# Kernel tuning notes

Measured on AMD Instinct MI355X. Metric: run time of the kernel, lower is better.

Reference implementation:

```python
import jax, jax.numpy as jnp
import numpy as np

B, T, C, H = 256, 256, 384, 64
MAX_REL = 3  # max_relative_position hardcoded in module


def setup_inputs() -> dict:
    key = jax.random.key(0)
    ks = jax.random.split(key, 6)
    s = 1.0 / np.sqrt(C)
    return {
        "x": jax.random.normal(ks[0], (B, T, C), dtype=jnp.float32),
        "Wq": jax.random.normal(ks[1], (C, H), dtype=jnp.float32) * s,
        "Wk": jax.random.normal(ks[2], (C, H), dtype=jnp.float32) * s,
        "Wv": jax.random.normal(ks[3], (C, H), dtype=jnp.float32) * s,
        "rel_k_table": jax.random.normal(ks[4], (2 * MAX_REL + 1, H), dtype=jnp.float32) * s,
        "rel_v_table": jax.random.normal(ks[5], (2 * MAX_REL + 1, H), dtype=jnp.float32) * s,
    }


def reference(x, Wq, Wk, Wv, rel_k_table, rel_v_table):
    Bd, Td, Cd = x.shape
    Hd = Wq.shape[1]
    q = x @ Wq  # [B,T,H]
    k = x @ Wk
    v = x @ Wv
    # relative position indices, clipped Shaw-style
    r = jnp.arange(Td)
    idx = jnp.clip(r[None, :] - r[:, None], -MAX_REL, MAX_REL) + MAX_REL  # [T,T]
    rk = rel_k_table[idx]  # [T,T,H]
    rv = rel_v_table[idx]  # [T,T,H]
    attn1 = jnp.einsum('bth,bsh->bts', q, k)
    attn2 = jnp.einsum('bth,tsh->bts', q, rk)
    scale = jnp.sqrt(jnp.asarray(Hd, dtype=x.dtype))
    scores = (attn1 + attn2) / scale
    causal = jnp.tril(jnp.ones((Td, Td), dtype=bool))
    scores = jnp.where(causal[None, :, :], scores, -jnp.inf)
    attn = jax.nn.softmax(scores, axis=-1)  # dropout = identity (eval mode)
    w1 = jnp.einsum('bts,bsh->bth', attn, v)
    w2 = jnp.einsum('bts,tsh->bth', attn, rv)
    return w1 + w2  # [B,T,H]
```

## Files before the change

### kernel.cpp

```cpp
#include <hip/hip_runtime.h>
#include <hip/hip_bf16.h>


typedef __attribute__((ext_vector_type(8))) __bf16 bf16x8;
typedef __attribute__((ext_vector_type(8))) short short8;
typedef __attribute__((ext_vector_type(4))) float f32x4;
typedef __attribute__((ext_vector_type(4))) int   i32x4;

#define MFMA16(A, B, C) __builtin_amdgcn_mfma_f32_16x16x32_bf16((A), (B), (C), 0, 0, 0)

__device__ __forceinline__ unsigned short f2bf(float f) {
    unsigned int u = __builtin_bit_cast(unsigned int, f);
    u = (u + 0x7FFFu + ((u >> 16) & 1u)) >> 16;
    return (unsigned short)u;
}
__device__ __forceinline__ float bf2f(unsigned short s) {
    unsigned int u = ((unsigned int)s) << 16;
    return __builtin_bit_cast(float, u);
}
__device__ __forceinline__ bf16x8 ld16(const unsigned short* p) {
    return __builtin_bit_cast(bf16x8, *(const i32x4*)p);
}

__global__ void prep_wt(const float* __restrict__ Wq, const float* __restrict__ Wk,
                        const float* __restrict__ Wv, unsigned short* __restrict__ Wt) {
    int i = blockIdx.x * 256 + threadIdx.x;
    if (i >= 3 * 64 * 384) return;
    int kk = i % 384;
    int h  = (i / 384) & 63;
    int w  = i / (384 * 64);
    const float* W = (w == 0) ? Wq : ((w == 1) ? Wk : Wv);
    Wt[i] = f2bf(W[kk * 64 + h]);
}

__global__ __launch_bounds__(512) void qkv_kernel(
        const float* __restrict__ x, const unsigned short* __restrict__ Wt,
        unsigned short* __restrict__ q, unsigned short* __restrict__ k,
        unsigned short* __restrict__ vT) {
    __shared__ unsigned short wlds[192][136];

    const int tid  = threadIdx.x;
    const int wave = tid >> 6;
    const int lane = tid & 63;
    const int c    = lane & 15;
    const int quad = lane >> 4;
    const int M0   = blockIdx.x * 128;
    const int myrow = M0 + wave * 16 + c;

    f32x4 zero = {0.f, 0.f, 0.f, 0.f};
    f32x4 aq[4], ak[4], av[4];
#pragma unroll
    for (int i = 0; i < 4; i++) { aq[i] = zero; ak[i] = zero; av[i] = zero; }

    for (int ck = 0; ck < 3; ck++) {
        if (ck) __syncthreads();
#pragma unroll
        for (int it = 0; it < 6; it++) {
            int i = it * 512 + tid;
            int r = i >> 4, kc = i & 15;
            i32x4 d = *(const i32x4*)(Wt + r * 384 + ck * 128 + kc * 8);
            *(i32x4*)(&wlds[r][kc * 8]) = d;
        }
        __syncthreads();

#pragma unroll
        for (int ks = 0; ks < 4; ks++) {
            const float* xp = x + (size_t)myrow * 384 + ck * 128 + ks * 32 + quad * 8;
            f32x4 x0 = *(const f32x4*)xp;
            f32x4 x1 = *(const f32x4*)(xp + 4);
            short8 xs;
#pragma unroll
            for (int j = 0; j < 4; j++) {
                xs[j]     = (short)f2bf(x0[j]);
                xs[4 + j] = (short)f2bf(x1[j]);
            }
            bf16x8 a = __builtin_bit_cast(bf16x8, xs);

#pragma unroll
            for (int nt = 0; nt < 8; nt++) {
                bf16x8 b = ld16(&wlds[nt * 16 + c][ks * 32 + quad * 8]);
                if (nt < 4) aq[nt]     = MFMA16(a, b, aq[nt]);
                else        ak[nt - 4] = MFMA16(a, b, ak[nt - 4]);
            }
#pragma unroll
            for (int mt = 0; mt < 4; mt++) {
                bf16x8 aw = ld16(&wlds[128 + mt * 16 + c][ks * 32 + quad * 8]);
                av[mt] = MFMA16(aw, a, av[mt]);
            }
        }
    }

    const int b   = M0 >> 8;
    const int t0b = M0 & 255;
#pragma unroll
    for (int nt = 0; nt < 4; nt++) {
#pragma unroll
        for (int r = 0; r < 4; r++) {
            int row = M0 + wave * 16 + quad * 4 + r;
            q[row * 64 + nt * 16 + c] = f2bf(aq[nt][r]);
            k[row * 64 + nt * 16 + c] = f2bf(ak[nt][r]);
        }
    }
#pragma unroll
    for (int mt = 0; mt < 4; mt++) {
#pragma unroll
        for (int r = 0; r < 4; r++) {
            int h = mt * 16 + quad * 4 + r;
            vT[(b * 64 + h) * 256 + t0b + wave * 16 + c] = f2bf(av[mt][r]);
        }
    }
}

__global__ __launch_bounds__(256) void attn_kernel(
        const unsigned short* __restrict__ q, const unsigned short* __restrict__ k,
        const unsigned short* __restrict__ vT,
        const float* __restrict__ relk, const float* __restrict__ relv,
        float* __restrict__ out) {
    __shared__ unsigned short P[64][264];
    __shared__ float E[64][4];

    const int tid  = threadIdx.x;
    const int wave = tid >> 6;
    const int lane = tid & 63;
    const int c    = lane & 15;
    const int quad = lane >> 4;
    const int tt   = blockIdx.x;
    const int b    = blockIdx.y;
    const int t0   = tt * 64;
    const int nst  = 4 * (tt + 1);

    {
        int r = tid >> 2, j = tid & 3;
        const unsigned short* qr = q + (size_t)(b * 256 + t0 + r) * 64;
        const float* rk = relk + j * 64;
        float e = 0.f;
#pragma unroll
        for (int hh = 0; hh < 64; hh += 8) {
            i32x4 d = *(const i32x4*)(qr + hh);
            const unsigned short* u = (const unsigned short*)&d;
#pragma unroll
            for (int j2 = 0; j2 < 8; j2++) e += bf2f(u[j2]) * rk[hh + j2];
        }
        E[r][j] = e;
    }
    __syncthreads();

    const unsigned short* qp = q + (size_t)(b * 256 + t0 + wave * 16 + c) * 64 + quad * 8;
    bf16x8 aq0 = ld16(qp);
    bf16x8 aq1 = ld16(qp + 32);

    f32x4 s[16];
    f32x4 zero = {0.f, 0.f, 0.f, 0.f};
#pragma unroll
    for (int st = 0; st < 16; st++) s[st] = zero;
#pragma unroll
    for (int st = 0; st < 16; st++) {
        if (st < nst) {
            const unsigned short* kp = k + (size_t)(b * 256 + st * 16 + c) * 64 + quad * 8;
            s[st] = MFMA16(aq0, ld16(kp), s[st]);
            s[st] = MFMA16(aq1, ld16(kp + 32), s[st]);
        }
    }

    const int rbase = wave * 16 + quad * 4;
    f32x4 ef[4];
#pragma unroll
    for (int r = 0; r < 4; r++) ef[r] = *(const f32x4*)(&E[rbase + r][0]);

    float m[4] = {-3.0e38f, -3.0e38f, -3.0e38f, -3.0e38f};
#pragma unroll
    for (int st = 0; st < 16; st++) {
        if (st < nst) {
#pragma unroll
            for (int r = 0; r < 4; r++) {
                int tl = rbase + r;
                int d  = st * 16 + c - (t0 + tl);
                float e  = (d <= -3) ? ef[r][0] : (d == -2) ? ef[r][1]
                         : (d == -1) ? ef[r][2] : ef[r][3];
                float sc = (d > 0) ? -1.0e30f : 0.125f * (s[st][r] + e);
                s[st][r] = sc;
                m[r] = fmaxf(m[r], sc);
            }
        }
    }
#pragma unroll
    for (int r = 0; r < 4; r++)
#pragma unroll
        for (int ofs = 1; ofs < 16; ofs <<= 1)
            m[r] = fmaxf(m[r], __shfl_xor(m[r], ofs, 64));

    float l[4] = {0.f, 0.f, 0.f, 0.f};
#pragma unroll
    for (int st = 0; st < 16; st++) {
        if (st < nst) {
#pragma unroll
            for (int r = 0; r < 4; r++) {
                float p = __expf(s[st][r] - m[r]);
                s[st][r] = p;
                l[r] += p;
            }
        }
    }
#pragma unroll
    for (int r = 0; r < 4; r++)
#pragma unroll
        for (int ofs = 1; ofs < 16; ofs <<= 1)
            l[r] += __shfl_xor(l[r], ofs, 64);
    float rl[4];
#pragma unroll
    for (int r = 0; r < 4; r++) rl[r] = 1.0f / l[r];

#pragma unroll
    for (int st = 0; st < 16; st++) {
        if (st < nst) {
#pragma unroll
            for (int r = 0; r < 4; r++)
                P[rbase + r][st * 16 + c] = f2bf(s[st][r] * rl[r]);
        }
    }
    __syncthreads();

    f32x4 o[4];
#pragma unroll
    for (int nt = 0; nt < 4; nt++) o[nt] = zero;
    const int ksteps = nst >> 1;
#pragma unroll
    for (int ks = 0; ks < 8; ks++) {
        if (ks < ksteps) {
            bf16x8 ap = ld16(&P[wave * 16 + c][ks * 32 + quad * 8]);
#pragma unroll
            for (int nt = 0; nt < 4; nt++) {
                const unsigned short* vp = vT + (size_t)(b * 64 + nt * 16 + c) * 256
                                              + ks * 32 + quad * 8;
                o[nt] = MFMA16(ap, ld16(vp), o[nt]);
            }
        }
    }

#pragma unroll
    for (int r = 0; r < 4; r++) {
        int tl = rbase + r;
        int tg = t0 + tl;
        int ia = (tg >= 2) ? tg - 2 : 0;
        int ib = (tg >= 1) ? tg - 1 : 0;
        float pa = (tg >= 2) ? bf2f(P[tl][ia]) : 0.f;
        float pb = (tg >= 1) ? bf2f(P[tl][ib]) : 0.f;
        float pc = bf2f(P[tl][tg]);
#pragma unroll
        for (int nt = 0; nt < 4; nt++) {
            int h = nt * 16 + c;
            float r0 = relv[h], r1 = relv[64 + h], r2 = relv[128 + h], r3 = relv[192 + h];
            float w2 = r0 + pa * (r1 - r0) + pb * (r2 - r0) + pc * (r3 - r0);
            out[(size_t)(b * 256 + tg) * 64 + h] = o[nt][r] + w2;
        }
    }
}

extern "C" void kernel_launch(void* const* d_in, const int* in_sizes, int n_in,
                              void* d_out, int out_size, void* d_ws, size_t ws_size,
                              hipStream_t stream) {
    const float* x    = (const float*)d_in[0];
    const float* Wq   = (const float*)d_in[1];
    const float* Wk   = (const float*)d_in[2];
    const float* Wv   = (const float*)d_in[3];
    const float* relk = (const float*)d_in[4];
    const float* relv = (const float*)d_in[5];
    float* out = (float*)d_out;

    char* ws = (char*)d_ws;
    unsigned short* q  = (unsigned short*)(ws);
    unsigned short* kk = (unsigned short*)(ws + 8388608);
    unsigned short* vT = (unsigned short*)(ws + 16777216);
    unsigned short* Wt = (unsigned short*)(ws + 25165824);

    prep_wt<<<288, 256, 0, stream>>>(Wq, Wk, Wv, Wt);
    qkv_kernel<<<512, 512, 0, stream>>>(x, Wt, q, kk, vT);
    attn_kernel<<<dim3(4, 256), 256, 0, stream>>>(q, kk, vT, relk, relv, out);
}
```

Baseline: 225.9 us.

## Fuse QKV projection and attention into one per-batch kernel with LDS-resident Q/K/V

Merges the QKV projection and attention kernels into a single kernel where each block handles one batch element. It computes Q, K and V for all 256 tokens into LDS and then loops over the four query tiles. This removes the global-memory round trip for the bf16 Q/K/V intermediates and one kernel launch. In exchange, each block needs about 142 KB of dynamic LDS, and only 256 blocks run with one block per CU. Each wave also holds a large accumulator set (48 f32x4 registers), which risks low occupancy and serialises the causal tiles inside one block.

```diff
diff --git a/kernel.cpp b/kernel.cpp
--- a/kernel.cpp
+++ b/kernel.cpp
@@ -33,105 +33,81 @@
     Wt[i] = f2bf(W[kk * 64 + h]);
 }
 
-__global__ __launch_bounds__(512) void qkv_kernel(
+__global__ __launch_bounds__(256, 1) void fused_kernel(
         const float* __restrict__ x, const unsigned short* __restrict__ Wt,
-        unsigned short* __restrict__ q, unsigned short* __restrict__ k,
-        unsigned short* __restrict__ vT) {
-    __shared__ unsigned short wlds[192][136];
+        const float* __restrict__ relk, const float* __restrict__ relv,
+        float* __restrict__ out) {
+    extern __shared__ char smem[];
+    unsigned short* qs = (unsigned short*)(smem);
+    unsigned short* kl = (unsigned short*)(smem + 36864);
+    unsigned short* vs = (unsigned short*)(smem + 73728);
+    unsigned short* P  = (unsigned short*)(smem + 107520);
+    float*          E  = (float*)(smem + 141312);
 
     const int tid  = threadIdx.x;
     const int wave = tid >> 6;
     const int lane = tid & 63;
     const int c    = lane & 15;
     const int quad = lane >> 4;
-    const int M0   = blockIdx.x * 128;
-    const int myrow = M0 + wave * 16 + c;
+    const int b    = blockIdx.x;
 
     f32x4 zero = {0.f, 0.f, 0.f, 0.f};
-    f32x4 aq[4], ak[4], av[4];
-#pragma unroll
-    for (int i = 0; i < 4; i++) { aq[i] = zero; ak[i] = zero; av[i] = zero; }
-
-    for (int ck = 0; ck < 3; ck++) {
-        if (ck) __syncthreads();
-#pragma unroll
-        for (int it = 0; it < 6; it++) {
-            int i = it * 512 + tid;
-            int r = i >> 4, kc = i & 15;
-            i32x4 d = *(const i32x4*)(Wt + r * 384 + ck * 128 + kc * 8);
-            *(i32x4*)(&wlds[r][kc * 8]) = d;
-        }
-        __syncthreads();
-
-#pragma unroll
-        for (int ks = 0; ks < 4; ks++) {
-            const float* xp = x + (size_t)myrow * 384 + ck * 128 + ks * 32 + quad * 8;
+
+    f32x4 accq[4][4], acck[4][4], accv[4][4];
+#pragma unroll
+    for (int i = 0; i < 4; i++)
+#pragma unroll
+        for (int j = 0; j < 4; j++) { accq[i][j] = zero; acck[i][j] = zero; accv[i][j] = zero; }
+
+    const float* xb = x + (size_t)b * 256 * 384;
+#pragma unroll
+    for (int kc = 0; kc < 12; kc++) {
+        const int ko = kc * 32 + quad * 8;
+        bf16x8 a[4];
+#pragma unroll
+        for (int mt = 0; mt < 4; mt++) {
+            const float* xp = xb + (wave * 64 + mt * 16 + c) * 384 + ko;
             f32x4 x0 = *(const f32x4*)xp;
             f32x4 x1 = *(const f32x4*)(xp + 4);
             short8 xs;
 #pragma unroll
-            for (int j = 0; j < 4; j++) {
-                xs[j]     = (short)f2bf(x0[j]);
-                xs[4 + j] = (short)f2bf(x1[j]);
-            }
-            bf16x8 a = __builtin_bit_cast(bf16x8, xs);
-
-#pragma unroll
-            for (int nt = 0; nt < 8; nt++) {
-                bf16x8 b = ld16(&wlds[nt * 16 + c][ks * 32 + quad * 8]);
-                if (nt < 4) aq[nt]     = MFMA16(a, b, aq[nt]);
-                else        ak[nt - 4] = MFMA16(a, b, ak[nt - 4]);
-            }
-#pragma unroll
-            for (int mt = 0; mt < 4; mt++) {
-                bf16x8 aw = ld16(&wlds[128 + mt * 16 + c][ks * 32 + quad * 8]);
-                av[mt] = MFMA16(aw, a, av[mt]);
-            }
-        }
+            for (int j = 0; j < 4; j++) { xs[j] = (short)f2bf(x0[j]); xs[4 + j] = (short)f2bf(x1[j]); }
+            a[mt] = __builtin_bit_cast(bf16x8, xs);
+        }
+        bf16x8 bq[4], bk[4], aw[4];
+#pragma unroll
+        for (int nt = 0; nt < 4; nt++) {
+            bq[nt] = ld16(Wt + (nt * 16 + c) * 384 + ko);
+            bk[nt] = ld16(Wt + (64 + nt * 16 + c) * 384 + ko);
+            aw[nt] = ld16(Wt + (128 + nt * 16 + c) * 384 + ko);
+        }
+#pragma unroll
+        for (int mt = 0; mt < 4; mt++)
+#pragma unroll
+            for (int nt = 0; nt < 4; nt++) {
+                accq[mt][nt] = MFMA16(a[mt], bq[nt], accq[mt][nt]);
+                acck[mt][nt] = MFMA16(a[mt], bk[nt], acck[mt][nt]);
+                accv[nt][mt] = MFMA16(aw[nt], a[mt], accv[nt][mt]);
+            }
     }
-
-    const int b   = M0 >> 8;
-    const int t0b = M0 & 255;
-#pragma unroll
-    for (int nt = 0; nt < 4; nt++) {
-#pragma unroll
-        for (int r = 0; r < 4; r++) {
-            int row = M0 + wave * 16 + quad * 4 + r;
-            q[row * 64 + nt * 16 + c] = f2bf(aq[nt][r]);
-            k[row * 64 + nt * 16 + c] = f2bf(ak[nt][r]);
-        }
-    }
-#pragma unroll
-    for (int mt = 0; mt < 4; mt++) {
-#pragma unroll
-        for (int r = 0; r < 4; r++) {
-            int h = mt * 16 + quad * 4 + r;
-            vT[(b * 64 + h) * 256 + t0b + wave * 16 + c] = f2bf(av[mt][r]);
-        }
-    }
-}
-
-__global__ __launch_bounds__(256) void attn_kernel(
-        const unsigned short* __restrict__ q, const unsigned short* __restrict__ k,
-        const unsigned short* __restrict__ vT,
-        const float* __restrict__ relk, const float* __restrict__ relv,
-        float* __restrict__ out) {
-    __shared__ unsigned short P[64][264];
-    __shared__ float E[64][4];
-
-    const int tid  = threadIdx.x;
-    const int wave = tid >> 6;
-    const int lane = tid & 63;
-    const int c    = lane & 15;
-    const int quad = lane >> 4;
-    const int tt   = blockIdx.x;
-    const int b    = blockIdx.y;
-    const int t0   = tt * 64;
-    const int nst  = 4 * (tt + 1);
-
-    {
-        int r = tid >> 2, j = tid & 3;
-        const unsigned short* qr = q + (size_t)(b * 256 + t0 + r) * 64;
+#pragma unroll
+    for (int mt = 0; mt < 4; mt++)
+#pragma unroll
+        for (int nt = 0; nt < 4; nt++)
+#pragma unroll
+            for (int r = 0; r < 4; r++) {
+                int row = wave * 64 + mt * 16 + quad * 4 + r;
+                qs[row * 72 + nt * 16 + c] = f2bf(accq[mt][nt][r]);
+                kl[row * 72 + nt * 16 + c] = f2bf(acck[mt][nt][r]);
+                vs[(nt * 16 + quad * 4 + r) * 264 + wave * 64 + mt * 16 + c] = f2bf(accv[nt][mt][r]);
+            }
+    __syncthreads();
+
+#pragma unroll
+    for (int it = 0; it < 4; it++) {
+        int rr = it * 64 + (tid >> 2);
+        int j  = tid & 3;
+        const unsigned short* qr = qs + rr * 72;
         const float* rk = relk + j * 64;
         float e = 0.f;
 #pragma unroll
@@ -141,118 +117,122 @@
 #pragma unroll
             for (int j2 = 0; j2 < 8; j2++) e += bf2f(u[j2]) * rk[hh + j2];
         }
-        E[r][j] = e;
+        E[rr * 4 + j] = e;
     }
     __syncthreads();
 
-    const unsigned short* qp = q + (size_t)(b * 256 + t0 + wave * 16 + c) * 64 + quad * 8;
-    bf16x8 aq0 = ld16(qp);
-    bf16x8 aq1 = ld16(qp + 32);
-
-    f32x4 s[16];
-    f32x4 zero = {0.f, 0.f, 0.f, 0.f};
-#pragma unroll
-    for (int st = 0; st < 16; st++) s[st] = zero;
-#pragma unroll
-    for (int st = 0; st < 16; st++) {
-        if (st < nst) {
-            const unsigned short* kp = k + (size_t)(b * 256 + st * 16 + c) * 64 + quad * 8;
-            s[st] = MFMA16(aq0, ld16(kp), s[st]);
-            s[st] = MFMA16(aq1, ld16(kp + 32), s[st]);
-        }
-    }
-
-    const int rbase = wave * 16 + quad * 4;
-    f32x4 ef[4];
-#pragma unroll
-    for (int r = 0; r < 4; r++) ef[r] = *(const f32x4*)(&E[rbase + r][0]);
-
-    float m[4] = {-3.0e38f, -3.0e38f, -3.0e38f, -3.0e38f};
-#pragma unroll
-    for (int st = 0; st < 16; st++) {
-        if (st < nst) {
-#pragma unroll
-            for (int r = 0; r < 4; r++) {
-                int tl = rbase + r;
-                int d  = st * 16 + c - (t0 + tl);
-                float e  = (d <= -3) ? ef[r][0] : (d == -2) ? ef[r][1]
-                         : (d == -1) ? ef[r][2] : ef[r][3];
-                float sc = (d > 0) ? -1.0e30f : 0.125f * (s[st][r] + e);
-                s[st][r] = sc;
-                m[r] = fmaxf(m[r], sc);
-            }
-        }
-    }
-#pragma unroll
-    for (int r = 0; r < 4; r++)
-#pragma unroll
-        for (int ofs = 1; ofs < 16; ofs <<= 1)
-            m[r] = fmaxf(m[r], __shfl_xor(m[r], ofs, 64));
-
-    float l[4] = {0.f, 0.f, 0.f, 0.f};
-#pragma unroll
-    for (int st = 0; st < 16; st++) {
-        if (st < nst) {
-#pragma unroll
-            for (int r = 0; r < 4; r++) {
-                float p = __expf(s[st][r] - m[r]);
-                s[st][r] = p;
-                l[r] += p;
-            }
-        }
-    }
-#pragma unroll
-    for (int r = 0; r < 4; r++)
-#pragma unroll
-        for (int ofs = 1; ofs < 16; ofs <<= 1)
-            l[r] += __shfl_xor(l[r], ofs, 64);
-    float rl[4];
-#pragma unroll
-    for (int r = 0; r < 4; r++) rl[r] = 1.0f / l[r];
-
-#pragma unroll
-    for (int st = 0; st < 16; st++) {
-        if (st < nst) {
-#pragma unroll
-            for (int r = 0; r < 4; r++)
-                P[rbase + r][st * 16 + c] = f2bf(s[st][r] * rl[r]);
-        }
-    }
-    __syncthreads();
-
-    f32x4 o[4];
-#pragma unroll
-    for (int nt = 0; nt < 4; nt++) o[nt] = zero;
-    const int ksteps = nst >> 1;
-#pragma unroll
-    for (int ks = 0; ks < 8; ks++) {
-        if (ks < ksteps) {
-            bf16x8 ap = ld16(&P[wave * 16 + c][ks * 32 + quad * 8]);
+    for (int tt = 0; tt < 4; tt++) {
+        const int t0  = tt * 64;
+        const int nst = 4 * (tt + 1);
+
+        const unsigned short* qp = qs + (t0 + wave * 16 + c) * 72 + quad * 8;
+        bf16x8 aq0 = ld16(qp);
+        bf16x8 aq1 = ld16(qp + 32);
+
+        f32x4 s[16];
+#pragma unroll
+        for (int st = 0; st < 16; st++) s[st] = zero;
+#pragma unroll
+        for (int st = 0; st < 16; st++) {
+            if (st < nst) {
+                const unsigned short* kp = kl + (st * 16 + c) * 72 + quad * 8;
+                s[st] = MFMA16(aq0, ld16(kp), s[st]);
+                s[st] = MFMA16(aq1, ld16(kp + 32), s[st]);
+            }
+        }
+
+        const int rbase = wave * 16 + quad * 4;
+        f32x4 ef[4];
+#pragma unroll
+        for (int r = 0; r < 4; r++) ef[r] = *(const f32x4*)(E + (t0 + rbase + r) * 4);
+
+        float m[4] = {-3.0e38f, -3.0e38f, -3.0e38f, -3.0e38f};
+#pragma unroll
+        for (int st = 0; st < 16; st++) {
+            if (st < nst) {
+#pragma unroll
+                for (int r = 0; r < 4; r++) {
+                    int tl = rbase + r;
+                    int d  = st * 16 + c - (t0 + tl);
+                    float e  = (d <= -3) ? ef[r][0] : (d == -2) ? ef[r][1]
+                             : (d == -1) ? ef[r][2] : ef[r][3];
+                    float sc = (d > 0) ? -1.0e30f : 0.125f * (s[st][r] + e);
+                    s[st][r] = sc;
+                    m[r] = fmaxf(m[r], sc);
+                }
+            }
+        }
+#pragma unroll
+        for (int r = 0; r < 4; r++)
+#pragma unroll
+            for (int ofs = 1; ofs < 16; ofs <<= 1)
+                m[r] = fmaxf(m[r], __shfl_xor(m[r], ofs, 64));
+
+        float l[4] = {0.f, 0.f, 0.f, 0.f};
+#pragma unroll
+        for (int st = 0; st < 16; st++) {
+            if (st < nst) {
+#pragma unroll
+                for (int r = 0; r < 4; r++) {
+                    float p = __expf(s[st][r] - m[r]);
+                    s[st][r] = p;
+                    l[r] += p;
+                }
+            }
+        }
+#pragma unroll
+        for (int r = 0; r < 4; r++)
+#pragma unroll
+            for (int ofs = 1; ofs < 16; ofs <<= 1)
+                l[r] += __shfl_xor(l[r], ofs, 64);
+        float rl[4];
+#pragma unroll
+        for (int r = 0; r < 4; r++) rl[r] = 1.0f / l[r];
+
+#pragma unroll
+        for (int st = 0; st < 16; st++) {
+            if (st < nst) {
+#pragma unroll
+                for (int r = 0; r < 4; r++)
+                    P[(rbase + r) * 264 + st * 16 + c] = f2bf(s[st][r] * rl[r]);
+            }
+        }
+        __syncthreads();
+
+        f32x4 o[4];
+#pragma unroll
+        for (int nt = 0; nt < 4; nt++) o[nt] = zero;
+        const int ksteps = nst >> 1;
+#pragma unroll
+        for (int ks = 0; ks < 8; ks++) {
+            if (ks < ksteps) {
+                bf16x8 ap = ld16(P + (wave * 16 + c) * 264 + ks * 32 + quad * 8);
+#pragma unroll
+                for (int nt = 0; nt < 4; nt++) {
+                    const unsigned short* vp = vs + (nt * 16 + c) * 264 + ks * 32 + quad * 8;
+                    o[nt] = MFMA16(ap, ld16(vp), o[nt]);
+                }
+            }
+        }
+
+#pragma unroll
+        for (int r = 0; r < 4; r++) {
+            int tl = rbase + r;
+            int tg = t0 + tl;
+            int ia = (tg >= 2) ? tg - 2 : 0;
+            int ib = (tg >= 1) ? tg - 1 : 0;
+            float pa = (tg >= 2) ? bf2f(P[tl * 264 + ia]) : 0.f;
+            float pb = (tg >= 1) ? bf2f(P[tl * 264 + ib]) : 0.f;
+            float pc = bf2f(P[tl * 264 + tg]);
 #pragma unroll
             for (int nt = 0; nt < 4; nt++) {
-                const unsigned short* vp = vT + (size_t)(b * 64 + nt * 16 + c) * 256
-                                              + ks * 32 + quad * 8;
-                o[nt] = MFMA16(ap, ld16(vp), o[nt]);
-            }
-        }
-    }
-
-#pragma unroll
-    for (int r = 0; r < 4; r++) {
-        int tl = rbase + r;
-        int tg = t0 + tl;
-        int ia = (tg >= 2) ? tg - 2 : 0;
-        int ib = (tg >= 1) ? tg - 1 : 0;
-        float pa = (tg >= 2) ? bf2f(P[tl][ia]) : 0.f;
-        float pb = (tg >= 1) ? bf2f(P[tl][ib]) : 0.f;
-        float pc = bf2f(P[tl][tg]);
-#pragma unroll
-        for (int nt = 0; nt < 4; nt++) {
-            int h = nt * 16 + c;
-            float r0 = relv[h], r1 = relv[64 + h], r2 = relv[128 + h], r3 = relv[192 + h];
-            float w2 = r0 + pa * (r1 - r0) + pb * (r2 - r0) + pc * (r3 - r0);
-            out[(size_t)(b * 256 + tg) * 64 + h] = o[nt][r] + w2;
-        }
+                int h = nt * 16 + c;
+                float r0 = relv[h], r1 = relv[64 + h], r2 = relv[128 + h], r3 = relv[192 + h];
+                float w2 = r0 + pa * (r1 - r0) + pb * (r2 - r0) + pc * (r3 - r0);
+                out[(size_t)(b * 256 + tg) * 64 + h] = o[nt][r] + w2;
+            }
+        }
+        __syncthreads();
     }
 }
 
@@ -267,13 +247,11 @@
     const float* relv = (const float*)d_in[5];
     float* out = (float*)d_out;
 
-    char* ws = (char*)d_ws;
-    unsigned short* q  = (unsigned short*)(ws);
-    unsigned short* kk = (unsigned short*)(ws + 8388608);
-    unsigned short* vT = (unsigned short*)(ws + 16777216);
-    unsigned short* Wt = (unsigned short*)(ws + 25165824);
+    unsigned short* Wt = (unsigned short*)d_ws;
+
+    (void)hipFuncSetAttribute((const void*)fused_kernel,
+                              hipFuncAttributeMaxDynamicSharedMemorySize, 145408);
 
     prep_wt<<<288, 256, 0, stream>>>(Wq, Wk, Wv, Wt);
-    qkv_kernel<<<512, 512, 0, stream>>>(x, Wt, q, kk, vT);
-    attn_kernel<<<dim3(4, 256), 256, 0, stream>>>(q, kk, vT, relk, relv, out);
-}
+    fused_kernel<<<256, 256, 145408, stream>>>(x, Wt, relk, relv, out);
+}
```

Result: faster. 212.9 us (-5.7%).

## Drop LDS staging of weights in QKV projection and read from global/L2

Applied to the files above, without the earlier changes.

The QKV projection kernel no longer stages the transposed bf16 weights into shared memory with block barriers. Each wave now loads weight fragments straight from global memory, relying on L2/L1 caching since all blocks share the small weight matrix. Blocks shrink to 256 threads with 64 rows each and the grid doubles. Both kernels get a min-blocks-per-SM launch bound of 3. This removes the LDS fill and sync overhead at the cost of redundant global weight reads per wave and possible register pressure from the occupancy hint.

```diff
diff --git a/kernel.cpp b/kernel.cpp
--- a/kernel.cpp
+++ b/kernel.cpp
@@ -33,85 +33,65 @@
     Wt[i] = f2bf(W[kk * 64 + h]);
 }
 
-__global__ __launch_bounds__(512) void qkv_kernel(
+__global__ __launch_bounds__(256, 3) void qkv_kernel(
         const float* __restrict__ x, const unsigned short* __restrict__ Wt,
         unsigned short* __restrict__ q, unsigned short* __restrict__ k,
         unsigned short* __restrict__ vT) {
-    __shared__ unsigned short wlds[192][136];
-
     const int tid  = threadIdx.x;
     const int wave = tid >> 6;
     const int lane = tid & 63;
     const int c    = lane & 15;
     const int quad = lane >> 4;
-    const int M0   = blockIdx.x * 128;
-    const int myrow = M0 + wave * 16 + c;
+    const int row0 = blockIdx.x * 64 + wave * 16;
 
     f32x4 zero = {0.f, 0.f, 0.f, 0.f};
     f32x4 aq[4], ak[4], av[4];
 #pragma unroll
     for (int i = 0; i < 4; i++) { aq[i] = zero; ak[i] = zero; av[i] = zero; }
 
-    for (int ck = 0; ck < 3; ck++) {
-        if (ck) __syncthreads();
-#pragma unroll
-        for (int it = 0; it < 6; it++) {
-            int i = it * 512 + tid;
-            int r = i >> 4, kc = i & 15;
-            i32x4 d = *(const i32x4*)(Wt + r * 384 + ck * 128 + kc * 8);
-            *(i32x4*)(&wlds[r][kc * 8]) = d;
-        }
-        __syncthreads();
-
-#pragma unroll
-        for (int ks = 0; ks < 4; ks++) {
-            const float* xp = x + (size_t)myrow * 384 + ck * 128 + ks * 32 + quad * 8;
-            f32x4 x0 = *(const f32x4*)xp;
-            f32x4 x1 = *(const f32x4*)(xp + 4);
-            short8 xs;
-#pragma unroll
-            for (int j = 0; j < 4; j++) {
-                xs[j]     = (short)f2bf(x0[j]);
-                xs[4 + j] = (short)f2bf(x1[j]);
-            }
-            bf16x8 a = __builtin_bit_cast(bf16x8, xs);
-
-#pragma unroll
-            for (int nt = 0; nt < 8; nt++) {
-                bf16x8 b = ld16(&wlds[nt * 16 + c][ks * 32 + quad * 8]);
-                if (nt < 4) aq[nt]     = MFMA16(a, b, aq[nt]);
-                else        ak[nt - 4] = MFMA16(a, b, ak[nt - 4]);
-            }
-#pragma unroll
-            for (int mt = 0; mt < 4; mt++) {
-                bf16x8 aw = ld16(&wlds[128 + mt * 16 + c][ks * 32 + quad * 8]);
-                av[mt] = MFMA16(aw, a, av[mt]);
-            }
-        }
-    }
-
-    const int b   = M0 >> 8;
-    const int t0b = M0 & 255;
+    const float* xp0 = x + (size_t)(row0 + c) * 384;
+
+#pragma unroll 2
+    for (int kc = 0; kc < 12; kc++) {
+        const int ko = kc * 32 + quad * 8;
+        f32x4 x0 = *(const f32x4*)(xp0 + ko);
+        f32x4 x1 = *(const f32x4*)(xp0 + ko + 4);
+        short8 xs;
+#pragma unroll
+        for (int j = 0; j < 4; j++) { xs[j] = (short)f2bf(x0[j]); xs[4 + j] = (short)f2bf(x1[j]); }
+        bf16x8 a = __builtin_bit_cast(bf16x8, xs);
+
+        bf16x8 bq[4], bk[4], aw[4];
+#pragma unroll
+        for (int nt = 0; nt < 4; nt++) {
+            bq[nt] = ld16(Wt + (nt * 16 + c) * 384 + ko);
+            bk[nt] = ld16(Wt + (64 + nt * 16 + c) * 384 + ko);
+            aw[nt] = ld16(Wt + (128 + nt * 16 + c) * 384 + ko);
+        }
+#pragma unroll
+        for (int nt = 0; nt < 4; nt++) {
+            aq[nt] = MFMA16(a, bq[nt], aq[nt]);
+            ak[nt] = MFMA16(a, bk[nt], ak[nt]);
+            av[nt] = MFMA16(aw[nt], a, av[nt]);
+        }
+    }
+
+    const int b   = row0 >> 8;
+    const int t0b = row0 & 255;
 #pragma unroll
     for (int nt = 0; nt < 4; nt++) {
 #pragma unroll
         for (int r = 0; r < 4; r++) {
-            int row = M0 + wave * 16 + quad * 4 + r;
+            int row = row0 + quad * 4 + r;
             q[row * 64 + nt * 16 + c] = f2bf(aq[nt][r]);
             k[row * 64 + nt * 16 + c] = f2bf(ak[nt][r]);
-        }
-    }
-#pragma unroll
-    for (int mt = 0; mt < 4; mt++) {
-#pragma unroll
-        for (int r = 0; r < 4; r++) {
-            int h = mt * 16 + quad * 4 + r;
-            vT[(b * 64 + h) * 256 + t0b + wave * 16 + c] = f2bf(av[mt][r]);
-        }
-    }
-}
-
-__global__ __launch_bounds__(256) void attn_kernel(
+            int h = nt * 16 + quad * 4 + r;
+            vT[(b * 64 + h) * 256 + t0b + c] = f2bf(av[nt][r]);
+        }
+    }
+}
+
+__global__ __launch_bounds__(256, 3) void attn_kernel(
         const unsigned short* __restrict__ q, const unsigned short* __restrict__ k,
         const unsigned short* __restrict__ vT,
         const float* __restrict__ relk, const float* __restrict__ relv,
@@ -274,6 +254,6 @@
     unsigned short* Wt = (unsigned short*)(ws + 25165824);
 
     prep_wt<<<288, 256, 0, stream>>>(Wq, Wk, Wv, Wt);
-    qkv_kernel<<<512, 512, 0, stream>>>(x, Wt, q, kk, vT);
+    qkv_kernel<<<1024, 256, 0, stream>>>(x, Wt, q, kk, vT);
     attn_kernel<<<dim3(4, 256), 256, 0, stream>>>(q, kk, vT, relk, relv, out);
 }
```

New measurement: 261.0 us. +15.5%, slower.

## Split attention into single-wave blocks with streaming softmax and MFMA rel-key bias

Applied to the files above, without the earlier changes.

Restructures the attention kernel from 256-thread blocks covering 64 query rows into 64-thread blocks covering 16 rows, launching 16x256 blocks. Causal tiles are skipped per block at finer granularity, and work is balanced by launching more small blocks. Softmax no longer subtracts the row max: exp is computed directly while streaming over key tiles and written unnormalized to LDS, with normalization applied at output. The relative-key bias is computed with MFMA against a bf16 padded rel_k table prepared in the prep kernel, and rel_v values are hoisted into registers. Dropping the max subtraction risks overflow for large scores, and bias precision drops to bf16.

```diff
diff --git a/kernel.cpp b/kernel.cpp
--- a/kernel.cpp
+++ b/kernel.cpp
@@ -23,14 +23,20 @@
 }
 
 __global__ void prep_wt(const float* __restrict__ Wq, const float* __restrict__ Wk,
-                        const float* __restrict__ Wv, unsigned short* __restrict__ Wt) {
+                        const float* __restrict__ Wv, const float* __restrict__ relk,
+                        unsigned short* __restrict__ Wt, unsigned short* __restrict__ Rk) {
     int i = blockIdx.x * 256 + threadIdx.x;
-    if (i >= 3 * 64 * 384) return;
-    int kk = i % 384;
-    int h  = (i / 384) & 63;
-    int w  = i / (384 * 64);
-    const float* W = (w == 0) ? Wq : ((w == 1) ? Wk : Wv);
-    Wt[i] = f2bf(W[kk * 64 + h]);
+    if (i < 3 * 64 * 384) {
+        int kk = i % 384;
+        int h  = (i / 384) & 63;
+        int w  = i / (384 * 64);
+        const float* W = (w == 0) ? Wq : ((w == 1) ? Wk : Wv);
+        Wt[i] = f2bf(W[kk * 64 + h]);
+    } else if (i < 3 * 64 * 384 + 1024) {
+        int j = i - 3 * 64 * 384;
+        int n = j >> 6, h = j & 63;
+        Rk[j] = (n < 4) ? f2bf(relk[n * 64 + h]) : (unsigned short)0;
+    }
 }
 
 __global__ __launch_bounds__(512) void qkv_kernel(
@@ -111,95 +117,71 @@
     }
 }
 
-__global__ __launch_bounds__(256) void attn_kernel(
+__global__ __launch_bounds__(64, 4) void attn_kernel(
         const unsigned short* __restrict__ q, const unsigned short* __restrict__ k,
-        const unsigned short* __restrict__ vT,
-        const float* __restrict__ relk, const float* __restrict__ relv,
-        float* __restrict__ out) {
-    __shared__ unsigned short P[64][264];
-    __shared__ float E[64][4];
-
-    const int tid  = threadIdx.x;
-    const int wave = tid >> 6;
-    const int lane = tid & 63;
+        const unsigned short* __restrict__ vT, const unsigned short* __restrict__ Rk,
+        const float* __restrict__ relv, float* __restrict__ out) {
+    __shared__ unsigned short P[16][264];
+    __shared__ float E[16][4];
+
+    const int lane = threadIdx.x;
     const int c    = lane & 15;
     const int quad = lane >> 4;
     const int tt   = blockIdx.x;
     const int b    = blockIdx.y;
-    const int t0   = tt * 64;
-    const int nst  = 4 * (tt + 1);
-
-    {
-        int r = tid >> 2, j = tid & 3;
-        const unsigned short* qr = q + (size_t)(b * 256 + t0 + r) * 64;
-        const float* rk = relk + j * 64;
-        float e = 0.f;
-#pragma unroll
-        for (int hh = 0; hh < 64; hh += 8) {
-            i32x4 d = *(const i32x4*)(qr + hh);
-            const unsigned short* u = (const unsigned short*)&d;
-#pragma unroll
-            for (int j2 = 0; j2 < 8; j2++) e += bf2f(u[j2]) * rk[hh + j2];
-        }
-        E[r][j] = e;
-    }
-    __syncthreads();
-
-    const unsigned short* qp = q + (size_t)(b * 256 + t0 + wave * 16 + c) * 64 + quad * 8;
+    const int t0   = tt * 16;
+    const int nst  = tt + 1;
+
+    f32x4 zero = {0.f, 0.f, 0.f, 0.f};
+
+    float rv[4][4];
+#pragma unroll
+    for (int j = 0; j < 4; j++)
+#pragma unroll
+        for (int nt = 0; nt < 4; nt++) rv[j][nt] = relv[j * 64 + nt * 16 + c];
+
+    const unsigned short* qp = q + (size_t)(b * 256 + t0 + c) * 64 + quad * 8;
     bf16x8 aq0 = ld16(qp);
     bf16x8 aq1 = ld16(qp + 32);
 
-    f32x4 s[16];
-    f32x4 zero = {0.f, 0.f, 0.f, 0.f};
-#pragma unroll
-    for (int st = 0; st < 16; st++) s[st] = zero;
+    {
+        f32x4 e = zero;
+        e = MFMA16(aq0, ld16(Rk + c * 64 + quad * 8), e);
+        e = MFMA16(aq1, ld16(Rk + c * 64 + 32 + quad * 8), e);
+        if (c < 4) {
+#pragma unroll
+            for (int r = 0; r < 4; r++) E[quad * 4 + r][c] = e[r];
+        }
+    }
+    __syncthreads();
+    f32x4 ef[4];
+#pragma unroll
+    for (int r = 0; r < 4; r++) ef[r] = *(const f32x4*)(&E[quad * 4 + r][0]);
+
+    float l[4] = {0.f, 0.f, 0.f, 0.f};
 #pragma unroll
     for (int st = 0; st < 16; st++) {
         if (st < nst) {
             const unsigned short* kp = k + (size_t)(b * 256 + st * 16 + c) * 64 + quad * 8;
-            s[st] = MFMA16(aq0, ld16(kp), s[st]);
-            s[st] = MFMA16(aq1, ld16(kp + 32), s[st]);
-        }
-    }
-
-    const int rbase = wave * 16 + quad * 4;
-    f32x4 ef[4];
-#pragma unroll
-    for (int r = 0; r < 4; r++) ef[r] = *(const f32x4*)(&E[rbase + r][0]);
-
-    float m[4] = {-3.0e38f, -3.0e38f, -3.0e38f, -3.0e38f};
-#pragma unroll
-    for (int st = 0; st < 16; st++) {
-        if (st < nst) {
+            f32x4 s = zero;
+            s = MFMA16(aq0, ld16(kp), s);
+            s = MFMA16(aq1, ld16(kp + 32), s);
 #pragma unroll
             for (int r = 0; r < 4; r++) {
-                int tl = rbase + r;
-                int d  = st * 16 + c - (t0 + tl);
-                float e  = (d <= -3) ? ef[r][0] : (d == -2) ? ef[r][1]
-                         : (d == -1) ? ef[r][2] : ef[r][3];
-                float sc = (d > 0) ? -1.0e30f : 0.125f * (s[st][r] + e);
-                s[st][r] = sc;
-                m[r] = fmaxf(m[r], sc);
-            }
-        }
-    }
-#pragma unroll
-    for (int r = 0; r < 4; r++)
-#pragma unroll
-        for (int ofs = 1; ofs < 16; ofs <<= 1)
-            m[r] = fmaxf(m[r], __shfl_xor(m[r], ofs, 64));
-
-    float l[4] = {0.f, 0.f, 0.f, 0.f};
-#pragma unroll
-    for (int st = 0; st < 16; st++) {
-        if (st < nst) {
-#pragma unroll
-            for (int r = 0; r < 4; r++) {
-                float p = __expf(s[st][r] - m[r]);
-                s[st][r] = p;
+                int tg = t0 + quad * 4 + r;
+                int sg = st * 16 + c;
+                int d  = sg - tg;
+                float e = (d <= -3) ? ef[r][0] : (d == -2) ? ef[r][1]
+                        : (d == -1) ? ef[r][2] : ef[r][3];
+                float p = (d > 0) ? 0.f : __expf(0.125f * (s[r] + e));
                 l[r] += p;
-            }
-        }
+                P[quad * 4 + r][sg] = f2bf(p);
+            }
+        }
+    }
+    if (nst & 1) {
+#pragma unroll
+        for (int r = 0; r < 4; r++) P[quad * 4 + r][nst * 16 + c] = 0;
     }
 #pragma unroll
     for (int r = 0; r < 4; r++)
@@ -209,25 +191,16 @@
     float rl[4];
 #pragma unroll
     for (int r = 0; r < 4; r++) rl[r] = 1.0f / l[r];
-
-#pragma unroll
-    for (int st = 0; st < 16; st++) {
-        if (st < nst) {
-#pragma unroll
-            for (int r = 0; r < 4; r++)
-                P[rbase + r][st * 16 + c] = f2bf(s[st][r] * rl[r]);
-        }
-    }
     __syncthreads();
 
     f32x4 o[4];
 #pragma unroll
     for (int nt = 0; nt < 4; nt++) o[nt] = zero;
-    const int ksteps = nst >> 1;
+    const int ksteps = (nst + 1) >> 1;
 #pragma unroll
     for (int ks = 0; ks < 8; ks++) {
         if (ks < ksteps) {
-            bf16x8 ap = ld16(&P[wave * 16 + c][ks * 32 + quad * 8]);
+            bf16x8 ap = ld16(&P[c][ks * 32 + quad * 8]);
 #pragma unroll
             for (int nt = 0; nt < 4; nt++) {
                 const unsigned short* vp = vT + (size_t)(b * 64 + nt * 16 + c) * 256
@@ -239,19 +212,17 @@
 
 #pragma unroll
     for (int r = 0; r < 4; r++) {
-        int tl = rbase + r;
+        int tl = quad * 4 + r;
         int tg = t0 + tl;
-        int ia = (tg >= 2) ? tg - 2 : 0;
-        int ib = (tg >= 1) ? tg - 1 : 0;
-        float pa = (tg >= 2) ? bf2f(P[tl][ia]) : 0.f;
-        float pb = (tg >= 1) ? bf2f(P[tl][ib]) : 0.f;
-        float pc = bf2f(P[tl][tg]);
+        float pa = (tg >= 2) ? bf2f(P[tl][tg - 2]) * rl[r] : 0.f;
+        float pb = (tg >= 1) ? bf2f(P[tl][tg - 1]) * rl[r] : 0.f;
+        float pc = bf2f(P[tl][tg]) * rl[r];
 #pragma unroll
         for (int nt = 0; nt < 4; nt++) {
-            int h = nt * 16 + c;
-            float r0 = relv[h], r1 = relv[64 + h], r2 = relv[128 + h], r3 = relv[192 + h];
-            float w2 = r0 + pa * (r1 - r0) + pb * (r2 - r0) + pc * (r3 - r0);
-            out[(size_t)(b * 256 + tg) * 64 + h] = o[nt][r] + w2;
+            float r0 = rv[0][nt];
+            float w2 = r0 + pa * (rv[1][nt] - r0) + pb * (rv[2][nt] - r0)
+                          + pc * (rv[3][nt] - r0);
+            out[(size_t)(b * 256 + tg) * 64 + nt * 16 + c] = o[nt][r] * rl[r] + w2;
         }
     }
 }
@@ -272,8 +243,9 @@
     unsigned short* kk = (unsigned short*)(ws + 8388608);
     unsigned short* vT = (unsigned short*)(ws + 16777216);
     unsigned short* Wt = (unsigned short*)(ws + 25165824);
-
-    prep_wt<<<288, 256, 0, stream>>>(Wq, Wk, Wv, Wt);
+    unsigned short* Rk = (unsigned short*)(ws + 25313280);
+
+    prep_wt<<<292, 256, 0, stream>>>(Wq, Wk, Wv, relk, Wt, Rk);
     qkv_kernel<<<512, 512, 0, stream>>>(x, Wt, q, kk, vT);
-    attn_kernel<<<dim3(4, 256), 256, 0, stream>>>(q, kk, vT, relk, relv, out);
-}
+    attn_kernel<<<dim3(16, 256), 64, 0, stream>>>(q, kk, vT, Rk, relv, out);
+}
```

Measured after the change: 208.5 us. 1.08x faster.
